# Optimization experiments

Hardware: AMD Instinct MI355X
Metric: run time of the kernel (lower is better)

## Reference

```python
import jax, jax.numpy as jnp
import numpy as np

TEMPERATURE = 1.0
N_NODES = 50000
N_EDGES = 1600000
BATCH = 2
C_IN = 64
C_OUT = 64


def setup_inputs() -> dict:
    key = jax.random.key(0)
    k = jax.random.split(key, 8)
    # edge_index with no self-loops: tgt = (src + 1 + off) % N, off in [0, N-2)
    src = jax.random.randint(k[0], (N_EDGES,), 0, N_NODES, dtype=jnp.int64)
    off = jax.random.randint(k[1], (N_EDGES,), 0, N_NODES - 1, dtype=jnp.int64)
    tgt = (src + 1 + off) % N_NODES
    edge_index = jnp.stack([src, tgt])  # (2, E)
    x = jax.random.normal(k[2], (BATCH, N_NODES, C_IN), dtype=jnp.float32)
    f_disc_orig = jax.random.uniform(k[3], (N_EDGES,), dtype=jnp.float32)
    fluxes = jax.random.normal(k[4], (BATCH, N_NODES), dtype=jnp.float32)
    W_conc = jax.random.normal(k[5], (C_OUT, C_IN), dtype=jnp.float32) * (1.0 / np.sqrt(C_IN))
    W_disc = jax.random.normal(k[6], (C_OUT, C_IN), dtype=jnp.float32) * (1.0 / np.sqrt(C_IN))
    bias = jnp.zeros((C_OUT,), dtype=jnp.float32)
    return {"x": x, "edge_index": edge_index, "f_disc_orig": f_disc_orig,
            "fluxes": fluxes, "W_conc": W_conc, "W_disc": W_disc, "bias": bias}


def reference(x, edge_index, f_disc_orig, fluxes, W_conc, W_disc, bias):
    B, N, _ = x.shape
    src0, tgt0 = edge_index[0], edge_index[1]  # original edges (no self-loops)
    loops = jnp.arange(N, dtype=edge_index.dtype)
    src = jnp.concatenate([src0, loops])  # (E+N,)
    tgt = jnp.concatenate([tgt0, loops])
    # GCN symmetric normalization D^{-1/2} A D^{-1/2} (with self-loops)
    deg = jnp.zeros((N,), x.dtype).at[tgt].add(1.0)
    dis = jnp.where(deg > 0, jax.lax.rsqrt(jnp.maximum(deg, 1e-30)), 0.0)
    norm = dis[src] * dis[tgt]  # (E+N,)
    # dynamic discordant strength on original (non-self-loop) edges
    sign_prod = jnp.tanh(fluxes[:, src0] * fluxes[:, tgt0] / TEMPERATURE)  # (B, E)
    keep = (1.0 + sign_prod) * 0.5
    fdo = f_disc_orig[None, :]
    f_disc = keep * fdo + (1.0 - keep) * (1.0 - fdo)  # (B, E)
    # self-loop messages are purely concordant (f_disc = 0)
    f_full = jnp.concatenate([f_disc, jnp.zeros((B, N), x.dtype)], axis=1)  # (B, E+N)
    # transform once per node, then gather per edge
    xc = jnp.einsum('bni,oi->bno', x, W_conc)  # (B, N, O)
    xd = jnp.einsum('bni,oi->bno', x, W_disc)
    msg = norm[None, :, None] * ((1.0 - f_full)[..., None] * xc[:, src] +
                                 f_full[..., None] * xd[:, src])  # (B, E+N, O)
    out = jnp.zeros((B, N, xc.shape[-1]), x.dtype).at[:, tgt].add(msg)
    return out + bias
```

## Files before the change

kernel.cpp:

```cpp
#include <hip/hip_runtime.h>
#include <math.h>


constexpr int C = 64;
constexpr int CNB = 128;
constexpr int CCAP = 5120;
constexpr int CHUNK = 4096;

typedef short short8 __attribute__((ext_vector_type(8)));
typedef float f32x4 __attribute__((ext_vector_type(4)));

__device__ __forceinline__ unsigned pack_bf16x2(float a, float b) {
    unsigned ua = __float_as_uint(a);
    ua = (ua + 0x7fffu + ((ua >> 16) & 1u)) >> 16;
    unsigned ub = __float_as_uint(b);
    ub = (ub + 0x7fffu + ((ub >> 16) & 1u)) >> 16;
    return ua | (ub << 16);
}
__device__ __forceinline__ float bflo(unsigned p) { return __uint_as_float(p << 16); }
__device__ __forceinline__ float bfhi(unsigned p) { return __uint_as_float(p & 0xffff0000u); }

__global__ __launch_bounds__(256) void convert_kernel(
    const float* __restrict__ x, unsigned* __restrict__ xb2, int nwords,
    int* __restrict__ coarseCursor, int ncoarse) {
    int i = blockIdx.x * blockDim.x + threadIdx.x;
    if (i < ncoarse) coarseCursor[i] = 0;
    int stride = gridDim.x * blockDim.x;
    const float2* x2 = (const float2*)x;
    for (int w = i; w < nwords; w += stride) {
        float2 xv = x2[w];
        xb2[w] = pack_bf16x2(xv.x, xv.y);
    }
}

__global__ __launch_bounds__(512) void binA1_kernel(
    const int* __restrict__ src, const int* __restrict__ tgt,
    const float* __restrict__ fdo, int* __restrict__ coarseCursor,
    unsigned long long* __restrict__ slab, int E, int ncoarse) {
    __shared__ int hcnt[512];
    __shared__ int hbase[512];
    const int tid = threadIdx.x;
    const int chunk0 = blockIdx.x * CHUNK;
    hcnt[tid] = 0;
    __syncthreads();
#pragma unroll 4
    for (int k = 0; k < CHUNK / 512; ++k) {
        int e = chunk0 + tid + k * 512;
        if (e < E) atomicAdd(&hcnt[tgt[e] >> 7], 1);
    }
    __syncthreads();
    {
        int cc = hcnt[tid];
        hbase[tid] = cc ? atomicAdd(&coarseCursor[tid & 511], cc) : 0;
        hcnt[tid] = 0;
    }
    __syncthreads();
#pragma unroll 4
    for (int k = 0; k < CHUNK / 512; ++k) {
        int e = chunk0 + tid + k * 512;
        if (e < E) {
            int t = tgt[e];
            int b = t >> 7;
            int pos = hbase[b] + atomicAdd(&hcnt[b], 1);
            if (pos < CCAP) {
                unsigned q = (unsigned)(fdo[e] * 32767.0f + 0.5f);
                unsigned long long en = (unsigned long long)(unsigned)src[e]
                                      | ((unsigned long long)(unsigned)(t & 127) << 17)
                                      | ((unsigned long long)q << 24);
                slab[(size_t)b * CCAP + pos] = en;
            }
        }
    }
}

__global__ __launch_bounds__(512) void binA2_kernel(
    const unsigned long long* __restrict__ slab,
    const int* __restrict__ coarseCursor, const float* __restrict__ flux,
    unsigned* __restrict__ epackFine, float4* __restrict__ nodeinfo, int N) {
    const int b = blockIdx.x;
    const int tid = threadIdx.x;
    __shared__ unsigned eout[CCAP];
    __shared__ int ncnt[CNB];
    __shared__ int nbase[CNB];
    __shared__ int ncur[CNB];
    int cnt = min(coarseCursor[b], CCAP);
    if (tid < CNB) { ncnt[tid] = 0; ncur[tid] = 0; }
    __syncthreads();
    const unsigned long long* sl = slab + (size_t)b * CCAP;
    for (int i = tid; i < cnt; i += 512)
        atomicAdd(&ncnt[(int)((sl[i] >> 17) & 127)], 1);
    __syncthreads();
    if (tid < 64) {
        int c0 = ncnt[2 * tid];
        int c1 = ncnt[2 * tid + 1];
        int s = c0 + c1;
        for (int off = 1; off < 64; off <<= 1) {
            int v = __shfl_up(s, off, 64);
            if (tid >= off) s += v;
        }
        nbase[2 * tid] = s - c1 - c0;
        nbase[2 * tid + 1] = s - c1;
    }
    __syncthreads();
    for (int i = tid; i < cnt; i += 512) {
        unsigned long long e = sl[i];
        int tl = (int)((e >> 17) & 127);
        int pos = nbase[tl] + atomicAdd(&ncur[tl], 1);
        eout[pos] = (unsigned)(e & 0x1FFFFull)
                  | ((unsigned)((e >> 24) & 0x7FFF) << 17);
    }
    if (tid < CNB) {
        int n = b * CNB + tid;
        if (n < N) {
            int dg = ncnt[tid];
            int rs = b * CCAP + nbase[tid];
            float4 ni;
            ni.x = rsqrtf((float)(dg + 1));
            ni.y = flux[n];
            ni.z = flux[N + n];
            ni.w = __int_as_float((dg << 21) | rs);
            nodeinfo[n] = ni;
        }
    }
    __syncthreads();
    unsigned* out = epackFine + (size_t)b * CCAP;
    for (int i = tid; i < cnt; i += 512) out[i] = eout[i];
}

__global__ __launch_bounds__(256) void aggregate_kernel(
    const float4* __restrict__ nodeinfo, const unsigned* __restrict__ epackFine,
    const unsigned* __restrict__ xb2, unsigned* __restrict__ up,
    unsigned* __restrict__ vp, int N) {
    const int lane = threadIdx.x & 63;
    const int wslot = threadIdx.x >> 6;
    const int node = blockIdx.x * 4 + wslot;
    __shared__ float4 s_e[4][2][64];
    if (node >= N) return;
    const int e2 = lane >> 4;
    const int q16 = lane & 15;
    const int g = q16 >> 3;
    const int p = q16 & 7;
    float4 ni = nodeinfo[node];
    const unsigned wbits = (unsigned)__float_as_int(ni.w);
    const int start = (int)(wbits & 0x1FFFFFu);
    const int end = start + (int)(wbits >> 21);
    const float dt = ni.x, f0t = ni.y, f1t = ni.z;
    const char* xbg = (const char*)xb2 + (size_t)g * N * 128 + p * 16;
    float au[8] = {0, 0, 0, 0, 0, 0, 0, 0};
    float av[8] = {0, 0, 0, 0, 0, 0, 0, 0};
    for (int base = start; base < end; base += 64) {
        int cnt = min(64, end - base);
        int cntp = (cnt + 7) & ~7;
        if (lane < cnt) {
            unsigned pe = epackFine[base + lane];
            int s = (int)(pe & 0x1FFFFu);
            float fd = (float)(pe >> 17) * (1.0f / 32767.0f);
            float4 nis = nodeinfo[s];
            float nrm = nis.x * dt;
            float p0 = nis.y * f0t;
            float p1 = nis.z * f1t;
            float k0 = 1.0f / (1.0f + __expf(-2.0f * p0));
            float k1 = 1.0f / (1.0f + __expf(-2.0f * p1));
            float w = 2.0f * fd - 1.0f;
            float f0 = fmaf(k0, w, 1.0f - fd);
            float f1 = fmaf(k1, w, 1.0f - fd);
            float soff = __int_as_float(s << 7);
            s_e[wslot][0][lane] = make_float4(soff, nrm * (1.0f - f0), nrm * f0, 0.f);
            s_e[wslot][1][lane] = make_float4(soff, nrm * (1.0f - f1), nrm * f1, 0.f);
        } else if (lane < cntp) {
            float4 z = make_float4(0.f, 0.f, 0.f, 0.f);
            s_e[wslot][0][lane] = z;
            s_e[wslot][1][lane] = z;
        }
        float4 rA = s_e[wslot][g][e2];
        float4 rB = s_e[wslot][g][4 + e2];
        uint4 xA = *(const uint4*)(xbg + __float_as_int(rA.x));
        uint4 xB = *(const uint4*)(xbg + __float_as_int(rB.x));
        for (int j = 8; j < cntp; j += 8) {
            float4 nA = s_e[wslot][g][j + e2];
            float4 nB = s_e[wslot][g][j + 4 + e2];
            uint4 pA = *(const uint4*)(xbg + __float_as_int(nA.x));
            uint4 pB = *(const uint4*)(xbg + __float_as_int(nB.x));
#pragma unroll
            for (int w = 0; w < 4; ++w) {
                unsigned xp = (&xA.x)[w];
                float lo = bflo(xp), hi = bfhi(xp);
                au[2 * w] = fmaf(rA.y, lo, au[2 * w]);
                au[2 * w + 1] = fmaf(rA.y, hi, au[2 * w + 1]);
                av[2 * w] = fmaf(rA.z, lo, av[2 * w]);
                av[2 * w + 1] = fmaf(rA.z, hi, av[2 * w + 1]);
                unsigned xq = (&xB.x)[w];
                float lo2 = bflo(xq), hi2 = bfhi(xq);
                au[2 * w] = fmaf(rB.y, lo2, au[2 * w]);
                au[2 * w + 1] = fmaf(rB.y, hi2, au[2 * w + 1]);
                av[2 * w] = fmaf(rB.z, lo2, av[2 * w]);
                av[2 * w + 1] = fmaf(rB.z, hi2, av[2 * w + 1]);
            }
            xA = pA; rA = nA;
            xB = pB; rB = nB;
        }
#pragma unroll
        for (int w = 0; w < 4; ++w) {
            unsigned xp = (&xA.x)[w];
            float lo = bflo(xp), hi = bfhi(xp);
            au[2 * w] = fmaf(rA.y, lo, au[2 * w]);
            au[2 * w + 1] = fmaf(rA.y, hi, au[2 * w + 1]);
            av[2 * w] = fmaf(rA.z, lo, av[2 * w]);
            av[2 * w + 1] = fmaf(rA.z, hi, av[2 * w + 1]);
            unsigned xq = (&xB.x)[w];
            float lo2 = bflo(xq), hi2 = bfhi(xq);
            au[2 * w] = fmaf(rB.y, lo2, au[2 * w]);
            au[2 * w + 1] = fmaf(rB.y, hi2, au[2 * w + 1]);
            av[2 * w] = fmaf(rB.z, lo2, av[2 * w]);
            av[2 * w + 1] = fmaf(rB.z, hi2, av[2 * w + 1]);
        }
    }
#pragma unroll
    for (int k = 0; k < 8; ++k) {
        au[k] += __shfl_xor(au[k], 16, 64);
        au[k] += __shfl_xor(au[k], 32, 64);
        av[k] += __shfl_xor(av[k], 16, 64);
        av[k] += __shfl_xor(av[k], 32, 64);
    }
    if (e2 == 0) {
        uint4 xs = *(const uint4*)(xbg + ((size_t)node << 7));
        float d2 = dt * dt;
#pragma unroll
        for (int w = 0; w < 4; ++w) {
            unsigned xp = (&xs.x)[w];
            au[2 * w] = fmaf(d2, bflo(xp), au[2 * w]);
            au[2 * w + 1] = fmaf(d2, bfhi(xp), au[2 * w + 1]);
        }
        uint4 uo, vo;
        uo.x = pack_bf16x2(au[0], au[1]);
        uo.y = pack_bf16x2(au[2], au[3]);
        uo.z = pack_bf16x2(au[4], au[5]);
        uo.w = pack_bf16x2(au[6], au[7]);
        vo.x = pack_bf16x2(av[0], av[1]);
        vo.y = pack_bf16x2(av[2], av[3]);
        vo.z = pack_bf16x2(av[4], av[5]);
        vo.w = pack_bf16x2(av[6], av[7]);
        size_t wo = ((size_t)(g * N + node)) * 32 + 4 * p;
        *(uint4*)(up + wo) = uo;
        *(uint4*)(vp + wo) = vo;
    }
}

__device__ __forceinline__ short8 make_bfrag(const float* __restrict__ row, int off) {
    const float4* p = (const float4*)(row + off);
    float4 lo = p[0], hi = p[1];
    uint4 w;
    w.x = pack_bf16x2(lo.x, lo.y);
    w.y = pack_bf16x2(lo.z, lo.w);
    w.z = pack_bf16x2(hi.x, hi.y);
    w.w = pack_bf16x2(hi.z, hi.w);
    return __builtin_bit_cast(short8, w);
}

__global__ __launch_bounds__(256) void gemm_mfma_kernel(
    const unsigned* __restrict__ up, const unsigned* __restrict__ vp,
    const float* __restrict__ Wc, const float* __restrict__ Wd,
    const float* __restrict__ bias, float* __restrict__ out, int ntiles) {
    const int lane = threadIdx.x & 63;
    const int nl = lane & 15;
    const int quad = lane >> 4;
    const int wave = blockIdx.x * 4 + (threadIdx.x >> 6);
    const int nwaves = gridDim.x * 4;

    short8 bf[4][4];
    float bt[4];
#pragma unroll
    for (int t = 0; t < 4; ++t) {
        int n = 16 * t + nl;
        const float* wcr = Wc + n * 64;
        const float* wdr = Wd + n * 64;
        bf[0][t] = make_bfrag(wcr, quad * 8);
        bf[1][t] = make_bfrag(wcr, 32 + quad * 8);
        bf[2][t] = make_bfrag(wdr, quad * 8);
        bf[3][t] = make_bfrag(wdr, 32 + quad * 8);
        bt[t] = bias[n];
    }

    for (int tile = wave; tile < ntiles; tile += nwaves) {
        int row = tile * 16 + nl;
        const uint4* ur = (const uint4*)(up + (size_t)row * 32);
        const uint4* vr = (const uint4*)(vp + (size_t)row * 32);
        short8 a0 = __builtin_bit_cast(short8, ur[quad]);
        short8 a1 = __builtin_bit_cast(short8, ur[4 + quad]);
        short8 a2 = __builtin_bit_cast(short8, vr[quad]);
        short8 a3 = __builtin_bit_cast(short8, vr[4 + quad]);
        f32x4 acc[4];
#pragma unroll
        for (int t = 0; t < 4; ++t) {
            f32x4 z = {0.f, 0.f, 0.f, 0.f};
            acc[t] = __builtin_amdgcn_mfma_f32_16x16x32_bf16(a0, bf[0][t], z, 0, 0, 0);
            acc[t] = __builtin_amdgcn_mfma_f32_16x16x32_bf16(a1, bf[1][t], acc[t], 0, 0, 0);
            acc[t] = __builtin_amdgcn_mfma_f32_16x16x32_bf16(a2, bf[2][t], acc[t], 0, 0, 0);
            acc[t] = __builtin_amdgcn_mfma_f32_16x16x32_bf16(a3, bf[3][t], acc[t], 0, 0, 0);
        }
        float* ob = out + ((size_t)(tile * 16 + quad * 4) << 6);
#pragma unroll
        for (int t = 0; t < 4; ++t) {
            int col = 16 * t + nl;
#pragma unroll
            for (int r = 0; r < 4; ++r)
                ob[(r << 6) + col] = acc[t][r] + bt[t];
        }
    }
}

extern "C" void kernel_launch(void* const* d_in, const int* in_sizes, int n_in,
                              void* d_out, int out_size, void* d_ws, size_t ws_size,
                              hipStream_t stream) {
    const float* x = (const float*)d_in[0];
    const int* ei = (const int*)d_in[1];
    const float* fdo = (const float*)d_in[2];
    const float* flux = (const float*)d_in[3];
    const float* Wc = (const float*)d_in[4];
    const float* Wd = (const float*)d_in[5];
    const float* bias = (const float*)d_in[6];
    float* out = (float*)d_out;

    const int E = in_sizes[2];
    const int BN = in_sizes[3];
    const int N = BN / 2;
    const int ncoarse = (N + CNB - 1) / CNB;

    auto align = [](size_t o) { return (o + 255) & ~(size_t)255; };
    char* ws = (char*)d_ws;
    size_t o = 0;
    int* coarseCursor = (int*)(ws + o);            o = align(o + (size_t)ncoarse * 4);
    float4* nodeinfo = (float4*)(ws + o);          o = align(o + (size_t)N * 16);
    unsigned long long* slab = (unsigned long long*)(ws + o);
    unsigned* up = (unsigned*)slab;
    o = align(o + (size_t)ncoarse * CCAP * 8);
    unsigned* epackFine = (unsigned*)(ws + o);     o = align(o + (size_t)ncoarse * CCAP * 4);
    unsigned* xb2 = (unsigned*)(ws + o);           o = align(o + (size_t)BN * 32 * 4);
    unsigned* vp = (unsigned*)(ws + o);            o += (size_t)BN * 32 * 4;

    const int* srcp = ei;
    const int* tgtp = ei + E;

    convert_kernel<<<2048, 256, 0, stream>>>(x, xb2, BN * 32, coarseCursor, ncoarse);
    binA1_kernel<<<(E + CHUNK - 1) / CHUNK, 512, 0, stream>>>(srcp, tgtp, fdo,
                                                              coarseCursor, slab, E, ncoarse);
    binA2_kernel<<<ncoarse, 512, 0, stream>>>(slab, coarseCursor, flux,
                                              epackFine, nodeinfo, N);
    aggregate_kernel<<<(N + 3) / 4, 256, 0, stream>>>(nodeinfo, epackFine, xb2,
                                                      up, vp, N);
    gemm_mfma_kernel<<<512, 256, 0, stream>>>(up, vp, Wc, Wd, bias, out, BN / 16);
}
```

Before: 210.5 us.

## Fuse aggregation with MFMA GEMM and merge bf16 conversion into binning kernel

```diff
diff --git a/kernel.cpp b/kernel.cpp
--- a/kernel.cpp
+++ b/kernel.cpp
@@ -20,23 +20,13 @@
 __device__ __forceinline__ float bflo(unsigned p) { return __uint_as_float(p << 16); }
 __device__ __forceinline__ float bfhi(unsigned p) { return __uint_as_float(p & 0xffff0000u); }
 
-__global__ __launch_bounds__(256) void convert_kernel(
-    const float* __restrict__ x, unsigned* __restrict__ xb2, int nwords,
-    int* __restrict__ coarseCursor, int ncoarse) {
-    int i = blockIdx.x * blockDim.x + threadIdx.x;
-    if (i < ncoarse) coarseCursor[i] = 0;
-    int stride = gridDim.x * blockDim.x;
-    const float2* x2 = (const float2*)x;
-    for (int w = i; w < nwords; w += stride) {
-        float2 xv = x2[w];
-        xb2[w] = pack_bf16x2(xv.x, xv.y);
-    }
-}
-
-__global__ __launch_bounds__(512) void binA1_kernel(
+__global__ __launch_bounds__(512) void binA1_convert_kernel(
     const int* __restrict__ src, const int* __restrict__ tgt,
     const float* __restrict__ fdo, int* __restrict__ coarseCursor,
-    unsigned long long* __restrict__ slab, int E, int ncoarse) {
+    unsigned long long* __restrict__ slab, int E, int ncoarse,
+    const float* __restrict__ x, unsigned* __restrict__ xb2, int nwords,
+    const float* __restrict__ Wc, const float* __restrict__ Wd,
+    unsigned* __restrict__ wpack) {
     __shared__ int hcnt[512];
     __shared__ int hbase[512];
     const int tid = threadIdx.x;
@@ -71,6 +61,21 @@
             }
         }
     }
+    int gid = blockIdx.x * 512 + tid;
+    int stride = gridDim.x * 512;
+    const float2* x2 = (const float2*)x;
+    for (int w = gid; w < nwords; w += stride) {
+        float2 xv = x2[w];
+        xb2[w] = pack_bf16x2(xv.x, xv.y);
+    }
+    const float2* wc2 = (const float2*)Wc;
+    const float2* wd2 = (const float2*)Wd;
+    for (int w = gid; w < 2048; w += stride) {
+        float2 a = wc2[w];
+        wpack[w] = pack_bf16x2(a.x, a.y);
+        float2 b = wd2[w];
+        wpack[2048 + w] = pack_bf16x2(b.x, b.y);
+    }
 }
 
 __global__ __launch_bounds__(512) void binA2_kernel(
@@ -127,24 +132,29 @@
     for (int i = tid; i < cnt; i += 512) out[i] = eout[i];
 }
 
-__global__ __launch_bounds__(256) void aggregate_kernel(
+__global__ __launch_bounds__(512) void agg_gemm_kernel(
     const float4* __restrict__ nodeinfo, const unsigned* __restrict__ epackFine,
-    const unsigned* __restrict__ xb2, unsigned* __restrict__ up,
-    unsigned* __restrict__ vp, int N) {
+    const unsigned* __restrict__ xb2, const unsigned* __restrict__ wpack,
+    const float* __restrict__ bias, float* __restrict__ out, int N) {
     const int lane = threadIdx.x & 63;
     const int wslot = threadIdx.x >> 6;
-    const int node = blockIdx.x * 4 + wslot;
-    __shared__ float4 s_e[4][2][64];
-    if (node >= N) return;
+    const int node = blockIdx.x * 8 + wslot;
+    __shared__ float4 s_e[8][2][64];
+    __shared__ unsigned arows[16][68];
     const int e2 = lane >> 4;
     const int q16 = lane & 15;
     const int g = q16 >> 3;
     const int p = q16 & 7;
-    float4 ni = nodeinfo[node];
-    const unsigned wbits = (unsigned)__float_as_int(ni.w);
-    const int start = (int)(wbits & 0x1FFFFFu);
-    const int end = start + (int)(wbits >> 21);
-    const float dt = ni.x, f0t = ni.y, f1t = ni.z;
+    const bool active = node < N;
+    int start = 0, end = 0;
+    float dt = 0.f, f0t = 0.f, f1t = 0.f;
+    if (active) {
+        float4 ni = nodeinfo[node];
+        const unsigned wbits = (unsigned)__float_as_int(ni.w);
+        start = (int)(wbits & 0x1FFFFFu);
+        end = start + (int)(wbits >> 21);
+        dt = ni.x; f0t = ni.y; f1t = ni.z;
+    }
     const char* xbg = (const char*)xb2 + (size_t)g * N * 128 + p * 16;
     float au[8] = {0, 0, 0, 0, 0, 0, 0, 0};
     float av[8] = {0, 0, 0, 0, 0, 0, 0, 0};
@@ -222,89 +232,60 @@
         av[k] += __shfl_xor(av[k], 16, 64);
         av[k] += __shfl_xor(av[k], 32, 64);
     }
+    const int r = wslot * 2 + g;
     if (e2 == 0) {
-        uint4 xs = *(const uint4*)(xbg + ((size_t)node << 7));
-        float d2 = dt * dt;
-#pragma unroll
-        for (int w = 0; w < 4; ++w) {
-            unsigned xp = (&xs.x)[w];
-            au[2 * w] = fmaf(d2, bflo(xp), au[2 * w]);
-            au[2 * w + 1] = fmaf(d2, bfhi(xp), au[2 * w + 1]);
-        }
-        uint4 uo, vo;
+        if (active) {
+            uint4 xs = *(const uint4*)(xbg + ((size_t)node << 7));
+            float d2 = dt * dt;
+#pragma unroll
+            for (int w = 0; w < 4; ++w) {
+                unsigned xp = (&xs.x)[w];
+                au[2 * w] = fmaf(d2, bflo(xp), au[2 * w]);
+                au[2 * w + 1] = fmaf(d2, bfhi(xp), au[2 * w + 1]);
+            }
+        }
+        uint4 uo;
         uo.x = pack_bf16x2(au[0], au[1]);
         uo.y = pack_bf16x2(au[2], au[3]);
         uo.z = pack_bf16x2(au[4], au[5]);
         uo.w = pack_bf16x2(au[6], au[7]);
+        *(uint4*)&arows[r][4 * p] = uo;
+    } else if (e2 == 1) {
+        uint4 vo;
         vo.x = pack_bf16x2(av[0], av[1]);
         vo.y = pack_bf16x2(av[2], av[3]);
         vo.z = pack_bf16x2(av[4], av[5]);
         vo.w = pack_bf16x2(av[6], av[7]);
-        size_t wo = ((size_t)(g * N + node)) * 32 + 4 * p;
-        *(uint4*)(up + wo) = uo;
-        *(uint4*)(vp + wo) = vo;
-    }
-}
-
-__device__ __forceinline__ short8 make_bfrag(const float* __restrict__ row, int off) {
-    const float4* p = (const float4*)(row + off);
-    float4 lo = p[0], hi = p[1];
-    uint4 w;
-    w.x = pack_bf16x2(lo.x, lo.y);
-    w.y = pack_bf16x2(lo.z, lo.w);
-    w.z = pack_bf16x2(hi.x, hi.y);
-    w.w = pack_bf16x2(hi.z, hi.w);
-    return __builtin_bit_cast(short8, w);
-}
-
-__global__ __launch_bounds__(256) void gemm_mfma_kernel(
-    const unsigned* __restrict__ up, const unsigned* __restrict__ vp,
-    const float* __restrict__ Wc, const float* __restrict__ Wd,
-    const float* __restrict__ bias, float* __restrict__ out, int ntiles) {
-    const int lane = threadIdx.x & 63;
-    const int nl = lane & 15;
-    const int quad = lane >> 4;
-    const int wave = blockIdx.x * 4 + (threadIdx.x >> 6);
-    const int nwaves = gridDim.x * 4;
-
-    short8 bf[4][4];
-    float bt[4];
-#pragma unroll
-    for (int t = 0; t < 4; ++t) {
-        int n = 16 * t + nl;
-        const float* wcr = Wc + n * 64;
-        const float* wdr = Wd + n * 64;
-        bf[0][t] = make_bfrag(wcr, quad * 8);
-        bf[1][t] = make_bfrag(wcr, 32 + quad * 8);
-        bf[2][t] = make_bfrag(wdr, quad * 8);
-        bf[3][t] = make_bfrag(wdr, 32 + quad * 8);
-        bt[t] = bias[n];
-    }
-
-    for (int tile = wave; tile < ntiles; tile += nwaves) {
-        int row = tile * 16 + nl;
-        const uint4* ur = (const uint4*)(up + (size_t)row * 32);
-        const uint4* vr = (const uint4*)(vp + (size_t)row * 32);
-        short8 a0 = __builtin_bit_cast(short8, ur[quad]);
-        short8 a1 = __builtin_bit_cast(short8, ur[4 + quad]);
-        short8 a2 = __builtin_bit_cast(short8, vr[quad]);
-        short8 a3 = __builtin_bit_cast(short8, vr[4 + quad]);
-        f32x4 acc[4];
-#pragma unroll
-        for (int t = 0; t < 4; ++t) {
-            f32x4 z = {0.f, 0.f, 0.f, 0.f};
-            acc[t] = __builtin_amdgcn_mfma_f32_16x16x32_bf16(a0, bf[0][t], z, 0, 0, 0);
-            acc[t] = __builtin_amdgcn_mfma_f32_16x16x32_bf16(a1, bf[1][t], acc[t], 0, 0, 0);
-            acc[t] = __builtin_amdgcn_mfma_f32_16x16x32_bf16(a2, bf[2][t], acc[t], 0, 0, 0);
-            acc[t] = __builtin_amdgcn_mfma_f32_16x16x32_bf16(a3, bf[3][t], acc[t], 0, 0, 0);
-        }
-        float* ob = out + ((size_t)(tile * 16 + quad * 4) << 6);
-#pragma unroll
-        for (int t = 0; t < 4; ++t) {
-            int col = 16 * t + nl;
-#pragma unroll
-            for (int r = 0; r < 4; ++r)
-                ob[(r << 6) + col] = acc[t][r] + bt[t];
+        *(uint4*)&arows[r][32 + 4 * p] = vo;
+    }
+    __syncthreads();
+    if (wslot < 4) {
+        const int nl = q16;
+        const int quad = e2;
+        const int n = 16 * wslot + nl;
+        const uint4* W4 = (const uint4*)wpack;
+        short8 b0 = __builtin_bit_cast(short8, W4[n * 8 + quad]);
+        short8 b1 = __builtin_bit_cast(short8, W4[n * 8 + 4 + quad]);
+        short8 b2 = __builtin_bit_cast(short8, W4[512 + n * 8 + quad]);
+        short8 b3 = __builtin_bit_cast(short8, W4[512 + n * 8 + 4 + quad]);
+        float bt = bias[n];
+        short8 a0 = __builtin_bit_cast(short8, *(const uint4*)&arows[nl][quad * 4]);
+        short8 a1 = __builtin_bit_cast(short8, *(const uint4*)&arows[nl][16 + quad * 4]);
+        short8 a2 = __builtin_bit_cast(short8, *(const uint4*)&arows[nl][32 + quad * 4]);
+        short8 a3 = __builtin_bit_cast(short8, *(const uint4*)&arows[nl][48 + quad * 4]);
+        f32x4 acc = {0.f, 0.f, 0.f, 0.f};
+        acc = __builtin_amdgcn_mfma_f32_16x16x32_bf16(a0, b0, acc, 0, 0, 0);
+        acc = __builtin_amdgcn_mfma_f32_16x16x32_bf16(a1, b1, acc, 0, 0, 0);
+        acc = __builtin_amdgcn_mfma_f32_16x16x32_bf16(a2, b2, acc, 0, 0, 0);
+        acc = __builtin_amdgcn_mfma_f32_16x16x32_bf16(a3, b3, acc, 0, 0, 0);
+        const int base8 = blockIdx.x * 8;
+#pragma unroll
+        for (int ri = 0; ri < 4; ++ri) {
+            int rl = quad * 4 + ri;
+            int nd = base8 + (rl >> 1);
+            if (nd < N)
+                out[((size_t)((rl & 1) * N + nd) << 6) + 16 * wslot + nl]
+                    = acc[ri] + bt;
         }
     }
 }
@@ -332,21 +313,20 @@
     int* coarseCursor = (int*)(ws + o);            o = align(o + (size_t)ncoarse * 4);
     float4* nodeinfo = (float4*)(ws + o);          o = align(o + (size_t)N * 16);
     unsigned long long* slab = (unsigned long long*)(ws + o);
-    unsigned* up = (unsigned*)slab;
     o = align(o + (size_t)ncoarse * CCAP * 8);
     unsigned* epackFine = (unsigned*)(ws + o);     o = align(o + (size_t)ncoarse * CCAP * 4);
     unsigned* xb2 = (unsigned*)(ws + o);           o = align(o + (size_t)BN * 32 * 4);
-    unsigned* vp = (unsigned*)(ws + o);            o += (size_t)BN * 32 * 4;
+    unsigned* wpack = (unsigned*)(ws + o);         o = align(o + 4096 * 4);
 
     const int* srcp = ei;
     const int* tgtp = ei + E;
 
-    convert_kernel<<<2048, 256, 0, stream>>>(x, xb2, BN * 32, coarseCursor, ncoarse);
-    binA1_kernel<<<(E + CHUNK - 1) / CHUNK, 512, 0, stream>>>(srcp, tgtp, fdo,
-                                                              coarseCursor, slab, E, ncoarse);
+    hipMemsetAsync(coarseCursor, 0, (size_t)ncoarse * 4, stream);
+    binA1_convert_kernel<<<(E + CHUNK - 1) / CHUNK, 512, 0, stream>>>(
+        srcp, tgtp, fdo, coarseCursor, slab, E, ncoarse,
+        x, xb2, BN * 32, Wc, Wd, wpack);
     binA2_kernel<<<ncoarse, 512, 0, stream>>>(slab, coarseCursor, flux,
                                               epackFine, nodeinfo, N);
-    aggregate_kernel<<<(N + 3) / 4, 256, 0, stream>>>(nodeinfo, epackFine, xb2,
-                                                      up, vp, N);
-    gemm_mfma_kernel<<<512, 256, 0, stream>>>(up, vp, Wc, Wd, bias, out, BN / 16);
-}
+    agg_gemm_kernel<<<(N + 7) / 8, 512, 0, stream>>>(nodeinfo, epackFine, xb2,
+                                                     wpack, bias, out, N);
+}
```

Result: slower. 215.5 us (+2.4%).

## Fuse bf16 conversion into binning kernel and split aggregation launch

Applied to the files above, without the earlier changes.

```diff
diff --git a/kernel.cpp b/kernel.cpp
--- a/kernel.cpp
+++ b/kernel.cpp
@@ -20,23 +20,11 @@
 __device__ __forceinline__ float bflo(unsigned p) { return __uint_as_float(p << 16); }
 __device__ __forceinline__ float bfhi(unsigned p) { return __uint_as_float(p & 0xffff0000u); }
 
-__global__ __launch_bounds__(256) void convert_kernel(
-    const float* __restrict__ x, unsigned* __restrict__ xb2, int nwords,
-    int* __restrict__ coarseCursor, int ncoarse) {
-    int i = blockIdx.x * blockDim.x + threadIdx.x;
-    if (i < ncoarse) coarseCursor[i] = 0;
-    int stride = gridDim.x * blockDim.x;
-    const float2* x2 = (const float2*)x;
-    for (int w = i; w < nwords; w += stride) {
-        float2 xv = x2[w];
-        xb2[w] = pack_bf16x2(xv.x, xv.y);
-    }
-}
-
-__global__ __launch_bounds__(512) void binA1_kernel(
+__global__ __launch_bounds__(512) void binA1_convert_kernel(
     const int* __restrict__ src, const int* __restrict__ tgt,
     const float* __restrict__ fdo, int* __restrict__ coarseCursor,
-    unsigned long long* __restrict__ slab, int E, int ncoarse) {
+    unsigned long long* __restrict__ slab, int E, int ncoarse,
+    const float* __restrict__ x, unsigned* __restrict__ xb2, int nwords) {
     __shared__ int hcnt[512];
     __shared__ int hbase[512];
     const int tid = threadIdx.x;
@@ -71,6 +59,13 @@
             }
         }
     }
+    int gid = blockIdx.x * 512 + tid;
+    int stride = gridDim.x * 512;
+    const float2* x2 = (const float2*)x;
+    for (int w = gid; w < nwords; w += stride) {
+        float2 xv = x2[w];
+        xb2[w] = pack_bf16x2(xv.x, xv.y);
+    }
 }
 
 __global__ __launch_bounds__(512) void binA2_kernel(
@@ -130,12 +125,12 @@
 __global__ __launch_bounds__(256) void aggregate_kernel(
     const float4* __restrict__ nodeinfo, const unsigned* __restrict__ epackFine,
     const unsigned* __restrict__ xb2, unsigned* __restrict__ up,
-    unsigned* __restrict__ vp, int N) {
+    unsigned* __restrict__ vp, int N, int nodeBase, int nodeEnd) {
     const int lane = threadIdx.x & 63;
     const int wslot = threadIdx.x >> 6;
-    const int node = blockIdx.x * 4 + wslot;
+    const int node = nodeBase + blockIdx.x * 4 + wslot;
     __shared__ float4 s_e[4][2][64];
-    if (node >= N) return;
+    if (node >= nodeEnd) return;
     const int e2 = lane >> 4;
     const int q16 = lane & 15;
     const int g = q16 >> 3;
@@ -341,12 +336,16 @@
     const int* srcp = ei;
     const int* tgtp = ei + E;
 
-    convert_kernel<<<2048, 256, 0, stream>>>(x, xb2, BN * 32, coarseCursor, ncoarse);
-    binA1_kernel<<<(E + CHUNK - 1) / CHUNK, 512, 0, stream>>>(srcp, tgtp, fdo,
-                                                              coarseCursor, slab, E, ncoarse);
+    const int H = ((N / 2) + 3) & ~3;
+
+    hipMemsetAsync(coarseCursor, 0, (size_t)ncoarse * 4, stream);
+    binA1_convert_kernel<<<(E + CHUNK - 1) / CHUNK, 512, 0, stream>>>(
+        srcp, tgtp, fdo, coarseCursor, slab, E, ncoarse, x, xb2, BN * 32);
     binA2_kernel<<<ncoarse, 512, 0, stream>>>(slab, coarseCursor, flux,
                                               epackFine, nodeinfo, N);
-    aggregate_kernel<<<(N + 3) / 4, 256, 0, stream>>>(nodeinfo, epackFine, xb2,
-                                                      up, vp, N);
+    aggregate_kernel<<<H / 4, 256, 0, stream>>>(nodeinfo, epackFine, xb2,
+                                                up, vp, N, 0, H);
+    aggregate_kernel<<<(N - H + 3) / 4, 256, 0, stream>>>(nodeinfo, epackFine, xb2,
+                                                          up, vp, N, H, N);
     gemm_mfma_kernel<<<512, 256, 0, stream>>>(up, vp, Wc, Wd, bias, out, BN / 16);
 }
```

New measurement: 214.3 us. No clear change (+1.8%).
